# Performance work log

Hardware: AMD Instinct MI355X
Metric: run time of the kernel (lower is better)

Reference implementation:

```python
import jax, jax.numpy as jnp
import numpy as np

NF4_LUT = jnp.array([-1.0, -0.6961928009986877, -0.5250730514526367, -0.39491719007492065,
                     -0.28444138169288635, -0.18477343022823334, -0.08820830285549164, 0.0,
                     0.07107656449079514, 0.14263366162776947, 0.22430233657360077,
                     0.3203405737876892, 0.4407068192958832, 0.5905631184577942,
                     0.796090841293335, 1.0], dtype=jnp.float32)

BLOCK_SIZE = 64
OUT_FEATURES = 11008
IN_FEATURES = 4096


def dequantize_nf4(packed, absmax, out_shape):
    # packed: (O, I//2) int codes 0..255; absmax: (O, num_blocks)
    higher = packed // 16
    lower = packed % 16
    unpacked = jnp.stack([lower, higher], axis=-1).reshape(out_shape)  # (O, I)
    dequant = NF4_LUT[unpacked]  # LUT gather -> fp32 (O, I)
    O, I = out_shape
    # block-wise absmax scale
    dequant = (dequant.reshape(O, I // BLOCK_SIZE, BLOCK_SIZE) * absmax[:, :, None]).reshape(O, I)
    return dequant


def setup_inputs() -> dict:
    key = jax.random.key(0)
    k1, k2, k3, k4 = jax.random.split(key, 4)
    x = jax.random.normal(k1, (4, 2048, IN_FEATURES), dtype=jnp.float32)
    weight = jax.random.randint(k2, (OUT_FEATURES, IN_FEATURES // 2), 0, 256, dtype=jnp.int32)
    absmax = jax.random.uniform(k3, (OUT_FEATURES, IN_FEATURES // BLOCK_SIZE), dtype=jnp.float32)
    bias = jax.random.normal(k4, (OUT_FEATURES,), dtype=jnp.float32)
    return {"x": x, "weight": weight, "absmax": absmax, "bias": bias}


def reference(x, weight, absmax, bias):
    w = dequantize_nf4(weight, absmax, (OUT_FEATURES, IN_FEATURES))  # (O, I)
    # F.linear: y = x @ w.T + bias
    return jnp.einsum('bsi,oi->bso', x, w) + bias
```

## Files before the change

### kernel.cpp

```cpp
#include <hip/hip_runtime.h>

#define IN_F 4096
#define OUT_F 11008

typedef __attribute__((ext_vector_type(8))) short bf16x8;
typedef __attribute__((ext_vector_type(4))) float f32x4;
typedef __attribute__((ext_vector_type(4))) unsigned short us4;
typedef __attribute__((ext_vector_type(8))) unsigned short us8;

__device__ __forceinline__ unsigned short f2bf(float f) {
  unsigned int u = __float_as_uint(f);
  u += 0x7FFFu + ((u >> 16) & 1u);
  return (unsigned short)(u >> 16);
}

__global__ __launch_bounds__(256) void cvt_x(const float* __restrict__ X,
                                             unsigned short* __restrict__ Xb, int n8) {
  for (int i = blockIdx.x * blockDim.x + threadIdx.x; i < n8;
       i += gridDim.x * blockDim.x) {
    const float4 a = reinterpret_cast<const float4*>(X)[2 * i];
    const float4 b = reinterpret_cast<const float4*>(X)[2 * i + 1];
    us8 h;
    h[0] = f2bf(a.x); h[1] = f2bf(a.y); h[2] = f2bf(a.z); h[3] = f2bf(a.w);
    h[4] = f2bf(b.x); h[5] = f2bf(b.y); h[6] = f2bf(b.z); h[7] = f2bf(b.w);
    reinterpret_cast<us8*>(Xb)[i] = h;
  }
}

__global__ __launch_bounds__(256) void dequant_w(const int* __restrict__ Wp,
                                                 const float* __restrict__ Amax,
                                                 unsigned short* __restrict__ Wb, int n4) {
  __shared__ float lutS[16];
  if (threadIdx.x < 16) {
    const float lut[16] = {-1.0f, -0.6961928009986877f, -0.5250730514526367f,
        -0.39491719007492065f, -0.28444138169288635f, -0.18477343022823334f,
        -0.08820830285549164f, 0.0f, 0.07107656449079514f, 0.14263366162776947f,
        0.22430233657360077f, 0.3203405737876892f, 0.4407068192958832f,
        0.5905631184577942f, 0.796090841293335f, 1.0f};
    lutS[threadIdx.x] = lut[threadIdx.x];
  }
  __syncthreads();
  for (int i = blockIdx.x * blockDim.x + threadIdx.x; i < n4;
       i += gridDim.x * blockDim.x) {
    const int j = i * 4;
    const int row = j >> 11;
    const int coli = j & 2047;
    const float am = Amax[row * (IN_F / 64) + (coli >> 5)];
    const int4 pk = reinterpret_cast<const int4*>(Wp)[i];
    us8 h; int c;
    c = pk.x & 255; h[0] = f2bf(lutS[c & 15] * am); h[1] = f2bf(lutS[c >> 4] * am);
    c = pk.y & 255; h[2] = f2bf(lutS[c & 15] * am); h[3] = f2bf(lutS[c >> 4] * am);
    c = pk.z & 255; h[4] = f2bf(lutS[c & 15] * am); h[5] = f2bf(lutS[c >> 4] * am);
    c = pk.w & 255; h[6] = f2bf(lutS[c & 15] * am); h[7] = f2bf(lutS[c >> 4] * am);
    reinterpret_cast<us8*>(Wb)[i] = h;
  }
}

#define MF(a, b, c) __builtin_amdgcn_mfma_f32_16x16x32_bf16(a, b, c, 0, 0, 0)
#define GLDS(src, dst) __builtin_amdgcn_global_load_lds( \
    (const __attribute__((address_space(1))) void*)(src), \
    (__attribute__((address_space(3))) void*)(dst), 16, 0, 0)
#define BAR __builtin_amdgcn_s_barrier()
#define VM4 asm volatile("s_waitcnt vmcnt(4)")
#define VM0 asm volatile("s_waitcnt vmcnt(0)")
#define P1 __builtin_amdgcn_s_setprio(1)
#define P0 __builtin_amdgcn_s_setprio(0)

__global__ __launch_bounds__(512, 2) void gemm256(
    const unsigned short* __restrict__ A,
    const unsigned short* __restrict__ B,
    const float* __restrict__ Bias, float* __restrict__ Out, int M) {
  extern __shared__ unsigned short sm[];
  char* const smc = (char*)sm;

  const int tid = threadIdx.x;
  const int l = tid & 63;
  const int wid = tid >> 6;

  const int Nb = OUT_F / 256;

  const int bps = 16 * Nb;
  const int pxc = bps >> 3;
  const int i6 = (int)blockIdx.x % bps;
  const int sup = (int)blockIdx.x / bps;
  const int k = (i6 & 7) * pxc + (i6 >> 3);
  const int m0 = (sup * 16 + (k & 15)) * 256;
  const int n0 = (k >> 4) * 256;

  const int lv = (l & 15) * 64 + (((l >> 4) ^ ((l >> 1) & 3)) * 16);
  const int aLane = (wid >> 2) * 8192 + lv;
  const int bLane = 32768 + (wid & 3) * 4096 + lv;

  const int rq = tid >> 2;
  const int cs = (tid & 3) ^ ((tid >> 3) & 3);
  const unsigned short* gAs = A + (size_t)(m0 + rq) * IN_F + cs * 8;
  const unsigned short* gBs = B + (size_t)(n0 + rq) * IN_F + cs * 8;

#define SA(t, kh) do { \
    unsigned short* d_ = sm + (size_t)((((t) & 1) * 4096) + (kh) * 1024 + wid * 64) * 8; \
    const unsigned short* s_ = gAs + (size_t)(t) * 64 + (kh) * 32; \
    GLDS(s_, d_); GLDS(s_ + 524288, d_ + 4096); } while (0)
#define SB(t, kh) do { \
    unsigned short* d_ = sm + (size_t)((((t) & 1) * 4096) + 2048 + (kh) * 1024 + wid * 64) * 8; \
    const unsigned short* s_ = gBs + (size_t)(t) * 64 + (kh) * 32; \
    GLDS(s_, d_); GLDS(s_ + 524288, d_ + 4096); } while (0)

#define MMQ(A0, A1, A2, A3, mb) do { \
    acc[(mb)+0][0]=MF(A0,y0,acc[(mb)+0][0]); acc[(mb)+0][1]=MF(A0,y1,acc[(mb)+0][1]); \
    acc[(mb)+0][2]=MF(A0,y2,acc[(mb)+0][2]); acc[(mb)+0][3]=MF(A0,y3,acc[(mb)+0][3]); \
    acc[(mb)+1][0]=MF(A1,y0,acc[(mb)+1][0]); acc[(mb)+1][1]=MF(A1,y1,acc[(mb)+1][1]); \
    acc[(mb)+1][2]=MF(A1,y2,acc[(mb)+1][2]); acc[(mb)+1][3]=MF(A1,y3,acc[(mb)+1][3]); \
    acc[(mb)+2][0]=MF(A2,y0,acc[(mb)+2][0]); acc[(mb)+2][1]=MF(A2,y1,acc[(mb)+2][1]); \
    acc[(mb)+2][2]=MF(A2,y2,acc[(mb)+2][2]); acc[(mb)+2][3]=MF(A2,y3,acc[(mb)+2][3]); \
    acc[(mb)+3][0]=MF(A3,y0,acc[(mb)+3][0]); acc[(mb)+3][1]=MF(A3,y1,acc[(mb)+3][1]); \
    acc[(mb)+3][2]=MF(A3,y2,acc[(mb)+3][2]); acc[(mb)+3][3]=MF(A3,y3,acc[(mb)+3][3]); } while (0)

#define KTILE(T, STG, VMW) do { \
    const char* LAb = smc + (((T) & 1) << 16) + aLane; \
    const char* LBb = smc + (((T) & 1) << 16) + bLane; \
    bf16x8 x0, x1, x2, x3, x4, x5, x6, x7, y0, y1, y2, y3; \
     \
    y0 = *(const bf16x8*)(LBb);        y1 = *(const bf16x8*)(LBb + 1024); \
    y2 = *(const bf16x8*)(LBb + 2048); y3 = *(const bf16x8*)(LBb + 3072); \
    x0 = *(const bf16x8*)(LAb);        x1 = *(const bf16x8*)(LAb + 1024); \
    x2 = *(const bf16x8*)(LAb + 2048); x3 = *(const bf16x8*)(LAb + 3072); \
    if (STG) SA((T) + 1, 0); \
    BAR; P1; MMQ(x0, x1, x2, x3, 0); P0; BAR; \
     \
    x4 = *(const bf16x8*)(LAb + 4096); x5 = *(const bf16x8*)(LAb + 5120); \
    x6 = *(const bf16x8*)(LAb + 6144); x7 = *(const bf16x8*)(LAb + 7168); \
    if (STG) SB((T) + 1, 0); \
    BAR; P1; MMQ(x4, x5, x6, x7, 4); P0; VMW; BAR; \
     \
    y0 = *(const bf16x8*)(LBb + 16384);        y1 = *(const bf16x8*)(LBb + 16384 + 1024); \
    y2 = *(const bf16x8*)(LBb + 16384 + 2048); y3 = *(const bf16x8*)(LBb + 16384 + 3072); \
    x0 = *(const bf16x8*)(LAb + 16384);        x1 = *(const bf16x8*)(LAb + 16384 + 1024); \
    x2 = *(const bf16x8*)(LAb + 16384 + 2048); x3 = *(const bf16x8*)(LAb + 16384 + 3072); \
    if (STG) SA((T) + 1, 1); \
    BAR; P1; MMQ(x0, x1, x2, x3, 0); P0; BAR; \
     \
    x4 = *(const bf16x8*)(LAb + 16384 + 4096); x5 = *(const bf16x8*)(LAb + 16384 + 5120); \
    x6 = *(const bf16x8*)(LAb + 16384 + 6144); x7 = *(const bf16x8*)(LAb + 16384 + 7168); \
    if (STG) SB((T) + 1, 1); \
    BAR; P1; MMQ(x4, x5, x6, x7, 4); P0; VMW; BAR; \
  } while (0)

  f32x4 acc[8][4];
#pragma unroll
  for (int i = 0; i < 8; ++i)
#pragma unroll
    for (int j = 0; j < 4; ++j) acc[i][j] = {0.f, 0.f, 0.f, 0.f};

  SA(0, 0); SB(0, 0); SA(0, 1); SB(0, 1);
  VM4;
  BAR;

  for (int T = 0; T < 63; ++T) { KTILE(T, 1, VM4); }
  KTILE(63, 0, VM0);

  const int crow = m0 + (wid >> 2) * 128 + ((l >> 4) << 2);
  const int ccol = n0 + (wid & 3) * 64 + (l & 15);
#pragma unroll
  for (int nf = 0; nf < 4; ++nf) {
    const float bv = Bias[ccol + nf * 16];
#pragma unroll
    for (int f = 0; f < 8; ++f)
#pragma unroll
      for (int rg = 0; rg < 4; ++rg)
        Out[(size_t)(crow + f * 16 + rg) * OUT_F + ccol + nf * 16] = acc[f][nf][rg] + bv;
  }
}

__global__ __launch_bounds__(256, 2) void nf4_gemm_fused(
    const float* __restrict__ X, const int* __restrict__ Wp,
    const float* __restrict__ Amax, const float* __restrict__ Bias,
    float* __restrict__ Out, int M) {
  __shared__ unsigned short As[128 * 64];
  __shared__ unsigned short Bs[128 * 64];
  __shared__ float lutS[16];

  const int t = threadIdx.x;
  const int l = t & 63;
  const int wid = t >> 6;

  if (t < 16) {
    const float lut[16] = {-1.0f, -0.6961928009986877f, -0.5250730514526367f,
        -0.39491719007492065f, -0.28444138169288635f, -0.18477343022823334f,
        -0.08820830285549164f, 0.0f, 0.07107656449079514f, 0.14263366162776947f,
        0.22430233657360077f, 0.3203405737876892f, 0.4407068192958832f,
        0.5905631184577942f, 0.796090841293335f, 1.0f};
    lutS[t] = lut[t];
  }

  const int ntile = OUT_F / 128;
  const int m0 = (blockIdx.x / ntile) * 128;
  const int n0 = (blockIdx.x % ntile) * 128;

  const int ar = t >> 4;
  const int ac4 = t & 15;
  const int br = t >> 3;
  const int bg = t & 7;
  const int wm = (wid >> 1) * 64;
  const int wn = (wid & 1) * 64;

  f32x4 acc[4][4];
#pragma unroll
  for (int i = 0; i < 4; ++i)
#pragma unroll
    for (int j = 0; j < 4; ++j) acc[i][j] = {0.f, 0.f, 0.f, 0.f};

  __syncthreads();

  for (int k0 = 0; k0 < IN_F; k0 += 64) {
#pragma unroll
    for (int p = 0; p < 8; ++p) {
      const int r = p * 16 + ar;
      const float4 v = *reinterpret_cast<const float4*>(
          X + (size_t)(m0 + r) * IN_F + k0 + ac4 * 4);
      us4 h;
      h[0] = f2bf(v.x); h[1] = f2bf(v.y); h[2] = f2bf(v.z); h[3] = f2bf(v.w);
      const int byte = r * 128 + ((ac4 * 8) ^ ((r & 7) << 4));
      *reinterpret_cast<us4*>(reinterpret_cast<char*>(As) + byte) = h;
    }
#pragma unroll
    for (int p = 0; p < 4; ++p) {
      const int r = p * 32 + br;
      const float amv = Amax[(size_t)(n0 + r) * (IN_F / 64) + (k0 >> 6)];
      const int4 pk = *reinterpret_cast<const int4*>(
          Wp + (size_t)(n0 + r) * (IN_F / 2) + (k0 >> 1) + bg * 4);
      us8 h;
      {
        int c;
        c = pk.x & 255; h[0] = f2bf(lutS[c & 15] * amv); h[1] = f2bf(lutS[c >> 4] * amv);
        c = pk.y & 255; h[2] = f2bf(lutS[c & 15] * amv); h[3] = f2bf(lutS[c >> 4] * amv);
        c = pk.z & 255; h[4] = f2bf(lutS[c & 15] * amv); h[5] = f2bf(lutS[c >> 4] * amv);
        c = pk.w & 255; h[6] = f2bf(lutS[c & 15] * amv); h[7] = f2bf(lutS[c >> 4] * amv);
      }
      const int byte = r * 128 + ((bg * 16) ^ ((r & 7) << 4));
      *reinterpret_cast<us8*>(reinterpret_cast<char*>(Bs) + byte) = h;
    }
    __syncthreads();

#pragma unroll
    for (int kk = 0; kk < 64; kk += 32) {
      bf16x8 af[4], bfv[4];
      const int kb = (kk + ((l >> 4) << 3)) * 2;
#pragma unroll
      for (int i = 0; i < 4; ++i) {
        const int row = wm + i * 16 + (l & 15);
        af[i] = *reinterpret_cast<const bf16x8*>(
            reinterpret_cast<const char*>(As) + row * 128 + (kb ^ ((row & 7) << 4)));
      }
#pragma unroll
      for (int j = 0; j < 4; ++j) {
        const int row = wn + j * 16 + (l & 15);
        bfv[j] = *reinterpret_cast<const bf16x8*>(
            reinterpret_cast<const char*>(Bs) + row * 128 + (kb ^ ((row & 7) << 4)));
      }
#pragma unroll
      for (int i = 0; i < 4; ++i)
#pragma unroll
        for (int j = 0; j < 4; ++j)
          acc[i][j] = __builtin_amdgcn_mfma_f32_16x16x32_bf16(af[i], bfv[j], acc[i][j], 0, 0, 0);
    }
    __syncthreads();
  }

  const int crow0 = m0 + wm + ((l >> 4) << 2);
  const int ccol0 = n0 + wn + (l & 15);
#pragma unroll
  for (int j = 0; j < 4; ++j) {
    const float bv = Bias[ccol0 + j * 16];
#pragma unroll
    for (int i = 0; i < 4; ++i)
#pragma unroll
      for (int rg = 0; rg < 4; ++rg)
        Out[(size_t)(crow0 + i * 16 + rg) * OUT_F + ccol0 + j * 16] = acc[i][j][rg] + bv;
  }
}

extern "C" void kernel_launch(void* const* d_in, const int* in_sizes, int n_in,
                              void* d_out, int out_size, void* d_ws, size_t ws_size,
                              hipStream_t stream) {
  const float* X = (const float*)d_in[0];
  const int* Wp = (const int*)d_in[1];
  const float* Amax = (const float*)d_in[2];
  const float* Bias = (const float*)d_in[3];
  float* Out = (float*)d_out;

  const int M = in_sizes[0] / IN_F;
  const size_t needX = (size_t)M * IN_F * 2;
  const size_t needW = (size_t)OUT_F * IN_F * 2;
  const int grid256 = (M / 256) * (OUT_F / 256);

  if (ws_size >= needX + needW && (M % 4096) == 0) {
    unsigned short* Xb = (unsigned short*)d_ws;
    unsigned short* Wb = Xb + (size_t)M * IN_F;
    (void)hipFuncSetAttribute(reinterpret_cast<const void*>(gemm256),
                              hipFuncAttributeMaxDynamicSharedMemorySize, 131072);
    cvt_x<<<2048, 256, 0, stream>>>(X, Xb, M * (IN_F / 8));
    dequant_w<<<2048, 256, 0, stream>>>(Wp, Amax, Wb, OUT_F * (IN_F / 8));
    gemm256<<<grid256, 512, 131072, stream>>>(Xb, Wb, Bias, Out, M);
  } else {
    const int grid = (M / 128) * (OUT_F / 128);
    nf4_gemm_fused<<<grid, 256, 0, stream>>>(X, Wp, Amax, Bias, Out, M);
  }
}
```

Baseline: 799.7 us.

## Switch GEMM inner loop to 32x32x16 bf16 MFMA tiles

Replaces the 16x16x32 MFMA micro-tiling with 32x32x16 MFMA instructions, restructuring the LDS read addressing, accumulator layout (4x2 f32x16) and epilogue store mapping. The larger MFMA tile reads fewer LDS fragments per FLOP and issues fewer MFMA instructions, aiming to cut LDS bandwidth and issue overhead. The K-tile loop is now split into two phases per tile, each of which issues both the A and B staging loads together. This changes barrier placement and may alter bank-conflict behaviour with the existing XOR swizzle.

```diff
diff --git a/kernel.cpp b/kernel.cpp
--- a/kernel.cpp
+++ b/kernel.cpp
@@ -4,6 +4,7 @@
 #define OUT_F 11008
 
 typedef __attribute__((ext_vector_type(8))) short bf16x8;
+typedef __attribute__((ext_vector_type(16))) float f32x16;
 typedef __attribute__((ext_vector_type(4))) float f32x4;
 typedef __attribute__((ext_vector_type(4))) unsigned short us4;
 typedef __attribute__((ext_vector_type(8))) unsigned short us8;
@@ -56,13 +57,14 @@
   }
 }
 
-#define MF(a, b, c) __builtin_amdgcn_mfma_f32_16x16x32_bf16(a, b, c, 0, 0, 0)
+#define MF32(a, b, c) __builtin_amdgcn_mfma_f32_32x32x16_bf16(a, b, c, 0, 0, 0)
 #define GLDS(src, dst) __builtin_amdgcn_global_load_lds( \
     (const __attribute__((address_space(1))) void*)(src), \
     (__attribute__((address_space(3))) void*)(dst), 16, 0, 0)
 #define BAR __builtin_amdgcn_s_barrier()
 #define VM4 asm volatile("s_waitcnt vmcnt(4)")
 #define VM0 asm volatile("s_waitcnt vmcnt(0)")
+#define VMNOP do {} while (0)
 #define P1 __builtin_amdgcn_s_setprio(1)
 #define P0 __builtin_amdgcn_s_setprio(0)
 
@@ -87,9 +89,11 @@
   const int m0 = (sup * 16 + (k & 15)) * 256;
   const int n0 = (k >> 4) * 256;
 
-  const int lv = (l & 15) * 64 + (((l >> 4) ^ ((l >> 1) & 3)) * 16);
-  const int aLane = (wid >> 2) * 8192 + lv;
-  const int bLane = 32768 + (wid & 3) * 4096 + lv;
+  const int r_l = l & 31;
+  const int g = l >> 5;
+  const int q = (g ^ ((r_l >> 1) & 3)) << 4;
+  const int aL = (wid >> 2) * 8192 + r_l * 64 + q;
+  const int bL = (wid & 3) * 4096 + r_l * 64 + q;
 
   const int rq = tid >> 2;
   const int cs = (tid & 3) ^ ((tid >> 3) & 3);
@@ -105,69 +109,58 @@
     const unsigned short* s_ = gBs + (size_t)(t) * 64 + (kh) * 32; \
     GLDS(s_, d_); GLDS(s_ + 524288, d_ + 4096); } while (0)
 
-#define MMQ(A0, A1, A2, A3, mb) do { \
-    acc[(mb)+0][0]=MF(A0,y0,acc[(mb)+0][0]); acc[(mb)+0][1]=MF(A0,y1,acc[(mb)+0][1]); \
-    acc[(mb)+0][2]=MF(A0,y2,acc[(mb)+0][2]); acc[(mb)+0][3]=MF(A0,y3,acc[(mb)+0][3]); \
-    acc[(mb)+1][0]=MF(A1,y0,acc[(mb)+1][0]); acc[(mb)+1][1]=MF(A1,y1,acc[(mb)+1][1]); \
-    acc[(mb)+1][2]=MF(A1,y2,acc[(mb)+1][2]); acc[(mb)+1][3]=MF(A1,y3,acc[(mb)+1][3]); \
-    acc[(mb)+2][0]=MF(A2,y0,acc[(mb)+2][0]); acc[(mb)+2][1]=MF(A2,y1,acc[(mb)+2][1]); \
-    acc[(mb)+2][2]=MF(A2,y2,acc[(mb)+2][2]); acc[(mb)+2][3]=MF(A2,y3,acc[(mb)+2][3]); \
-    acc[(mb)+3][0]=MF(A3,y0,acc[(mb)+3][0]); acc[(mb)+3][1]=MF(A3,y1,acc[(mb)+3][1]); \
-    acc[(mb)+3][2]=MF(A3,y2,acc[(mb)+3][2]); acc[(mb)+3][3]=MF(A3,y3,acc[(mb)+3][3]); } while (0)
-
-#define KTILE(T, STG, VMW) do { \
-    const char* LAb = smc + (((T) & 1) << 16) + aLane; \
-    const char* LBb = smc + (((T) & 1) << 16) + bLane; \
-    bf16x8 x0, x1, x2, x3, x4, x5, x6, x7, y0, y1, y2, y3; \
-     \
-    y0 = *(const bf16x8*)(LBb);        y1 = *(const bf16x8*)(LBb + 1024); \
-    y2 = *(const bf16x8*)(LBb + 2048); y3 = *(const bf16x8*)(LBb + 3072); \
-    x0 = *(const bf16x8*)(LAb);        x1 = *(const bf16x8*)(LAb + 1024); \
-    x2 = *(const bf16x8*)(LAb + 2048); x3 = *(const bf16x8*)(LAb + 3072); \
-    if (STG) SA((T) + 1, 0); \
-    BAR; P1; MMQ(x0, x1, x2, x3, 0); P0; BAR; \
-     \
-    x4 = *(const bf16x8*)(LAb + 4096); x5 = *(const bf16x8*)(LAb + 5120); \
-    x6 = *(const bf16x8*)(LAb + 6144); x7 = *(const bf16x8*)(LAb + 7168); \
-    if (STG) SB((T) + 1, 0); \
-    BAR; P1; MMQ(x4, x5, x6, x7, 4); P0; VMW; BAR; \
-     \
-    y0 = *(const bf16x8*)(LBb + 16384);        y1 = *(const bf16x8*)(LBb + 16384 + 1024); \
-    y2 = *(const bf16x8*)(LBb + 16384 + 2048); y3 = *(const bf16x8*)(LBb + 16384 + 3072); \
-    x0 = *(const bf16x8*)(LAb + 16384);        x1 = *(const bf16x8*)(LAb + 16384 + 1024); \
-    x2 = *(const bf16x8*)(LAb + 16384 + 2048); x3 = *(const bf16x8*)(LAb + 16384 + 3072); \
-    if (STG) SA((T) + 1, 1); \
-    BAR; P1; MMQ(x0, x1, x2, x3, 0); P0; BAR; \
-     \
-    x4 = *(const bf16x8*)(LAb + 16384 + 4096); x5 = *(const bf16x8*)(LAb + 16384 + 5120); \
-    x6 = *(const bf16x8*)(LAb + 16384 + 6144); x7 = *(const bf16x8*)(LAb + 16384 + 7168); \
-    if (STG) SB((T) + 1, 1); \
-    BAR; P1; MMQ(x4, x5, x6, x7, 4); P0; VMW; BAR; \
+#define PHASE(T, kh, STG, VMW) do { \
+    const char* LAb = smc + (((T) & 1) << 16) + (kh) * 16384; \
+    const char* LBb = LAb + 32768; \
+    bf16x8 a00, a01, a10, a11, a20, a21, a30, a31, b00, b01, b10, b11; \
+    a00 = *(const bf16x8*)(LAb + aL);          a01 = *(const bf16x8*)(LAb + (aL ^ 32)); \
+    a10 = *(const bf16x8*)(LAb + 2048 + aL);   a11 = *(const bf16x8*)(LAb + 2048 + (aL ^ 32)); \
+    a20 = *(const bf16x8*)(LAb + 4096 + aL);   a21 = *(const bf16x8*)(LAb + 4096 + (aL ^ 32)); \
+    a30 = *(const bf16x8*)(LAb + 6144 + aL);   a31 = *(const bf16x8*)(LAb + 6144 + (aL ^ 32)); \
+    b00 = *(const bf16x8*)(LBb + bL);          b01 = *(const bf16x8*)(LBb + (bL ^ 32)); \
+    b10 = *(const bf16x8*)(LBb + 2048 + bL);   b11 = *(const bf16x8*)(LBb + 2048 + (bL ^ 32)); \
+    if (STG) { SA((T) + 1, kh); SB((T) + 1, kh); } \
+    BAR; P1; \
+    acc[0][0] = MF32(a00, b00, acc[0][0]); acc[0][1] = MF32(a00, b10, acc[0][1]); \
+    acc[1][0] = MF32(a10, b00, acc[1][0]); acc[1][1] = MF32(a10, b10, acc[1][1]); \
+    acc[2][0] = MF32(a20, b00, acc[2][0]); acc[2][1] = MF32(a20, b10, acc[2][1]); \
+    acc[3][0] = MF32(a30, b00, acc[3][0]); acc[3][1] = MF32(a30, b10, acc[3][1]); \
+    acc[0][0] = MF32(a01, b01, acc[0][0]); acc[0][1] = MF32(a01, b11, acc[0][1]); \
+    acc[1][0] = MF32(a11, b01, acc[1][0]); acc[1][1] = MF32(a11, b11, acc[1][1]); \
+    acc[2][0] = MF32(a21, b01, acc[2][0]); acc[2][1] = MF32(a21, b11, acc[2][1]); \
+    acc[3][0] = MF32(a31, b01, acc[3][0]); acc[3][1] = MF32(a31, b11, acc[3][1]); \
+    P0; VMW; BAR; \
   } while (0)
 
-  f32x4 acc[8][4];
-#pragma unroll
-  for (int i = 0; i < 8; ++i)
-#pragma unroll
-    for (int j = 0; j < 4; ++j) acc[i][j] = {0.f, 0.f, 0.f, 0.f};
+  f32x16 acc[4][2];
+#pragma unroll
+  for (int i = 0; i < 4; ++i)
+#pragma unroll
+    for (int j = 0; j < 2; ++j)
+#pragma unroll
+      for (int r = 0; r < 16; ++r) acc[i][j][r] = 0.f;
 
   SA(0, 0); SB(0, 0); SA(0, 1); SB(0, 1);
   VM4;
   BAR;
 
-  for (int T = 0; T < 63; ++T) { KTILE(T, 1, VM4); }
-  KTILE(63, 0, VM0);
-
-  const int crow = m0 + (wid >> 2) * 128 + ((l >> 4) << 2);
-  const int ccol = n0 + (wid & 3) * 64 + (l & 15);
-#pragma unroll
-  for (int nf = 0; nf < 4; ++nf) {
-    const float bv = Bias[ccol + nf * 16];
-#pragma unroll
-    for (int f = 0; f < 8; ++f)
-#pragma unroll
-      for (int rg = 0; rg < 4; ++rg)
-        Out[(size_t)(crow + f * 16 + rg) * OUT_F + ccol + nf * 16] = acc[f][nf][rg] + bv;
+  for (int T = 0; T < 63; ++T) { PHASE(T, 0, 1, VM4); PHASE(T, 1, 1, VM4); }
+  PHASE(63, 0, 0, VM0);
+  PHASE(63, 1, 0, VMNOP);
+
+  const int crow = m0 + (wid >> 2) * 128;
+  const int ccol = n0 + (wid & 3) * 64 + (l & 31);
+  const int rbase = (l >> 5) * 4;
+#pragma unroll
+  for (int nt = 0; nt < 2; ++nt) {
+    const float bv = Bias[ccol + nt * 32];
+#pragma unroll
+    for (int mt = 0; mt < 4; ++mt)
+#pragma unroll
+      for (int r = 0; r < 16; ++r) {
+        const int row = crow + mt * 32 + (r & 3) + 8 * (r >> 2) + rbase;
+        Out[(size_t)row * OUT_F + ccol + nt * 32] = acc[mt][nt][r] + bv;
+      }
   }
 }
 
```

Measured after the change: 861.5 us. 1.08x slower.
